# Performance work log

Hardware: AMD Instinct MI355X
Metric: run time of the kernel (lower is better)

## Reference

```python
import jax, jax.numpy as jnp
import numpy as np
from jax import lax

L, C, NH, DFF = 4, 256, 8, 1024
H, W = 56, 56
N = H * W
TOPK, USENUM = 16, 10


def _conv3x3(x, w, b):
    # x: [B,Cin,H,W], w: [Cout,Cin,3,3]
    y = lax.conv_general_dilated(x, w, (1, 1), 'SAME',
                                 dimension_numbers=('NCHW', 'OIHW', 'NCHW'))
    return y + b[None, :, None, None]


def _ln(x, g, b, eps=1e-5):
    m = jnp.mean(x, axis=-1, keepdims=True)
    v = jnp.mean(jnp.square(x - m), axis=-1, keepdims=True)
    return (x - m) * lax.rsqrt(v + eps) * g + b


def _forward(src, conv1_w, conv1_b, conv2_w, conv2_b, near_emb,
             Wq, bq, Wk, bk, Wv, bv, Wo, bo, W1, b1, W2, b2,
             ln1_g, ln1_b, ln2_g, ln2_b, norm_g, norm_b):
    bs, c, h, w = src.shape  # bs == 1 (required by graph_pos broadcasting)
    n = h * w
    nh = NH
    dh = c // nh
    scale = dh ** -0.5

    # conv positional encoder -> per-head sigmoid map
    pe = jax.nn.sigmoid(_conv3x3(jax.nn.relu(_conv3x3(src, conv1_w, conv1_b)),
                                 conv2_w, conv2_b))          # [1,nh,h,w]
    gp = pe.reshape(bs, nh, n)[0].T                          # [n,nh]
    # graph_pos = |pe_i - pe_j| as additive attention bias, [nh,n,n]
    bias = jnp.abs(gp[:, None, :] - gp[None, :, :]).transpose(2, 0, 1)

    x = src.reshape(bs, c, n)[0].T                           # [n,c] tokens
    rows = jnp.arange(n)[:, None]

    for i in range(L):
        # ---- per-layer kNN graph on current features ----
        sq = jnp.sum(x * x, axis=1)
        d2 = sq[:, None] - 2.0 * (x @ x.T) + sq[None, :]     # [n,n] sq dists
        _, idx = lax.top_k(-d2, TOPK)                        # k nearest
        graph = jnp.zeros((n, n), x.dtype).at[rows, idx].set(1.0)
        near = jnp.sum(graph, axis=0)                        # in-degree [n]
        ni = (near / jnp.max(near) * (USENUM - 1)).astype(jnp.int32)
        pos = near_emb[ni]                                   # [n,c] embed gather

        # ---- attention (pos added to q,k; graph_pos biases logits) ----
        qk_in = x + pos
        q = (qk_in @ Wq[i].T + bq[i]).reshape(n, nh, dh)
        k = (qk_in @ Wk[i].T + bk[i]).reshape(n, nh, dh)
        v = (x @ Wv[i].T + bv[i]).reshape(n, nh, dh)
        s = jnp.einsum('ihd,jhd->hij', q * scale, k) + bias  # [nh,n,n]
        att = jax.nn.softmax(s, axis=-1)
        o = jnp.einsum('hij,jhd->ihd', att, v).reshape(n, c) @ Wo[i].T + bo[i]
        x = _ln(x + o, ln1_g[i], ln1_b[i])

        # ---- FFN ----
        ff = jax.nn.relu(x @ W1[i].T + b1[i]) @ W2[i].T + b2[i]
        x = _ln(x + ff, ln2_g[i], ln2_b[i])

    x = _ln(x, norm_g, norm_b)
    return x.T.reshape(bs, c, h, w)


def setup_inputs() -> dict:
    key = jax.random.key(0)
    ks = jax.random.split(key, 20)

    def rn(k, shape, s=0.02):
        return jax.random.normal(k, shape, jnp.float32) * s

    return {
        'src': jax.random.normal(ks[0], (1, C, H, W), jnp.float32),
        'conv1_w': rn(ks[1], (C // 2, C, 3, 3), 0.05),
        'conv1_b': jnp.zeros((C // 2,), jnp.float32),
        'conv2_w': rn(ks[2], (NH, C // 2, 3, 3), 0.05),
        'conv2_b': jnp.zeros((NH,), jnp.float32),
        'near_emb': rn(ks[3], (USENUM, C)),
        'Wq': rn(ks[4], (L, C, C)), 'bq': jnp.zeros((L, C), jnp.float32),
        'Wk': rn(ks[5], (L, C, C)), 'bk': jnp.zeros((L, C), jnp.float32),
        'Wv': rn(ks[6], (L, C, C)), 'bv': jnp.zeros((L, C), jnp.float32),
        'Wo': rn(ks[7], (L, C, C)), 'bo': jnp.zeros((L, C), jnp.float32),
        'W1': rn(ks[8], (L, DFF, C)), 'b1': jnp.zeros((L, DFF), jnp.float32),
        'W2': rn(ks[9], (L, C, DFF)), 'b2': jnp.zeros((L, C), jnp.float32),
        'ln1_g': jnp.ones((L, C), jnp.float32), 'ln1_b': jnp.zeros((L, C), jnp.float32),
        'ln2_g': jnp.ones((L, C), jnp.float32), 'ln2_b': jnp.zeros((L, C), jnp.float32),
        'norm_g': jnp.ones((C,), jnp.float32), 'norm_b': jnp.zeros((C,), jnp.float32),
    }


def reference(src, conv1_w, conv1_b, conv2_w, conv2_b, near_emb,
              Wq, bq, Wk, bk, Wv, bv, Wo, bo, W1, b1, W2, b2,
              ln1_g, ln1_b, ln2_g, ln2_b, norm_g, norm_b):
    return _forward(src, conv1_w, conv1_b, conv2_w, conv2_b, near_emb,
                    Wq, bq, Wk, bk, Wv, bv, Wo, bo, W1, b1, W2, b2,
                    ln1_g, ln1_b, ln2_g, ln2_b, norm_g, norm_b)
```

## Files before the change

kernel.cpp:

```cpp
#include <hip/hip_runtime.h>
#include <math.h>

#define N_TOK 3136
#define CD    256
#define NHD   8
#define DH    32
#define DFFD  1024
#define SCALE 0.17677669529663687f
#define LOG2E 1.4426950408889634f
#define QSC   (SCALE * LOG2E)

typedef __attribute__((ext_vector_type(8))) short short8v;
typedef __attribute__((ext_vector_type(4))) float f32x4;

__device__ __forceinline__ unsigned long long sx64(unsigned long long v, int m) {
  unsigned lo = (unsigned)__shfl_xor((int)(unsigned)(v & 0xffffffffull), m, 64);
  unsigned hi = (unsigned)__shfl_xor((int)(unsigned)(v >> 32), m, 64);
  return ((unsigned long long)hi << 32) | lo;
}

__device__ __forceinline__ unsigned f2mono(float v) {
  unsigned b = __float_as_uint(v);
  return (b & 0x80000000u) ? ~b : (b | 0x80000000u);
}

__device__ __forceinline__ short bfr(float f) {
  unsigned u = __float_as_uint(f);
  unsigned r = (u + 0x7fffu + ((u >> 16) & 1u)) >> 16;
  return (short)r;
}

__device__ __forceinline__ short8v cvt8(float4 a, float4 b) {
  short8v r;
  r[0] = bfr(a.x); r[1] = bfr(a.y); r[2] = bfr(a.z); r[3] = bfr(a.w);
  r[4] = bfr(b.x); r[5] = bfr(b.y); r[6] = bfr(b.z); r[7] = bfr(b.w);
  return r;
}

__global__ __launch_bounds__(256) void transpose_k(const float* __restrict__ in,
    float* __restrict__ out, int R, int C) {
  __shared__ float ls[32][33];
  const int c0 = blockIdx.x * 32, r0 = blockIdx.y * 32;
  const int tx = threadIdx.x & 31, ty = threadIdx.x >> 5;
#pragma unroll
  for (int j = 0; j < 4; ++j) {
    int r = ty + j * 8;
    ls[r][tx] = in[(size_t)(r0 + r) * C + c0 + tx];
  }
  __syncthreads();
#pragma unroll
  for (int j = 0; j < 4; ++j) {
    int cc = ty + j * 8;
    out[(size_t)(c0 + cc) * R + r0 + tx] = ls[tx][cc];
  }
}

__global__ __launch_bounds__(256) void wtr_k(const float* __restrict__ w,
                                             float* __restrict__ wt) {
  const int e = blockIdx.x * 256 + threadIdx.x;
  const int r = e >> 15;
  const int rem = e & 32767;
  const int co = rem >> 8, ci = rem & 255;
  wt[e] = w[((size_t)co * 256 + ci) * 9 + r];
}

__global__ __launch_bounds__(256) void conv1_k(const float* __restrict__ X,
    const float* __restrict__ WT, float* __restrict__ P) {
  __shared__ __align__(16) short As[32][40];
  __shared__ __align__(16) short Bs[64][40];
  const int n0 = blockIdx.x * 64;
  const int m0 = blockIdx.y * 32;
  const int ky = blockIdx.z;
  const int t = threadIdx.x;
  const int w = t >> 6, l = t & 63;
  const int g = l >> 4, c = l & 15;
  const int wr = w >> 1, wc = w & 1;
  const int sr = t >> 2, seg = t & 3;
  const int p = m0 + (sr & 31);
  const int y = p / 56, x = p - y * 56;
  const int yy = y + ky - 1;
  f32x4 acc[2] = {};
  for (int kx = 0; kx < 3; ++kx) {
    const int xx = x + kx - 1;
    const bool valid = (t < 128) && ((unsigned)yy < 56u) && ((unsigned)xx < 56u);
    const float* Ap = X + (size_t)(yy * 56 + xx) * CD + seg * 8;
    const float* Bp = WT + ((size_t)(ky * 3 + kx) * 128 + n0 + sr) * CD + seg * 8;
    for (int k0 = 0; k0 < CD; k0 += 32) {
      float4 a1 = make_float4(0.f, 0.f, 0.f, 0.f), a2 = a1;
      if (valid) { a1 = *(const float4*)(Ap + k0); a2 = *(const float4*)(Ap + k0 + 4); }
      const float4 b1 = *(const float4*)(Bp + k0);
      const float4 b2 = *(const float4*)(Bp + k0 + 4);
      __syncthreads();
      if (t < 128) *(short8v*)&As[sr][seg * 8] = cvt8(a1, a2);
      *(short8v*)&Bs[sr][seg * 8] = cvt8(b1, b2);
      __syncthreads();
      const short8v af = *(const short8v*)&As[wr * 16 + c][g * 8];
      const short8v bf0 = *(const short8v*)&Bs[wc * 32 + c][g * 8];
      const short8v bf1 = *(const short8v*)&Bs[wc * 32 + 16 + c][g * 8];
      acc[0] = __builtin_amdgcn_mfma_f32_16x16x32_bf16(af, bf0, acc[0], 0, 0, 0);
      acc[1] = __builtin_amdgcn_mfma_f32_16x16x32_bf16(af, bf1, acc[1], 0, 0, 0);
    }
  }
#pragma unroll
  for (int ni = 0; ni < 2; ++ni) {
    const int col = n0 + wc * 32 + ni * 16 + c;
#pragma unroll
    for (int q = 0; q < 4; ++q) {
      const int m = m0 + wr * 16 + g * 4 + q;
      P[((size_t)ky * N_TOK + m) * 128 + col] = acc[ni][q];
    }
  }
}

__global__ __launch_bounds__(256) void convred_k(const float* __restrict__ P,
    const float* __restrict__ b, float* __restrict__ T1) {
  const int e = blockIdx.x * 256 + threadIdx.x;
  const float v = P[e] + P[401408 + e] + P[802816 + e] + b[e & 127];
  T1[e] = fmaxf(v, 0.f);
}

template <int RELU>
__global__ __launch_bounds__(256) void gemm32_k(const float* __restrict__ A,
    const float* __restrict__ B, const float* __restrict__ bias,
    float* __restrict__ C, int N, int K) {
  __shared__ __align__(16) short As[32][40];
  __shared__ __align__(16) short Bs[64][40];
  const int n0 = blockIdx.x * 64;
  const int m0 = blockIdx.y * 32;
  const int t = threadIdx.x;
  const int w = t >> 6, l = t & 63;
  const int g = l >> 4, c = l & 15;
  const int wr = w >> 1, wc = w & 1;
  const int sr = t >> 2, seg = t & 3;
  const float* Ap = A + (size_t)(m0 + (sr & 31)) * K + seg * 8;
  const float* Bp = B + (size_t)(n0 + sr) * K + seg * 8;
  f32x4 acc[2] = {};
  for (int k0 = 0; k0 < K; k0 += 32) {
    float4 a1 = make_float4(0.f, 0.f, 0.f, 0.f), a2 = a1;
    if (t < 128) { a1 = *(const float4*)(Ap + k0); a2 = *(const float4*)(Ap + k0 + 4); }
    const float4 b1 = *(const float4*)(Bp + k0);
    const float4 b2 = *(const float4*)(Bp + k0 + 4);
    __syncthreads();
    if (t < 128) *(short8v*)&As[sr][seg * 8] = cvt8(a1, a2);
    *(short8v*)&Bs[sr][seg * 8] = cvt8(b1, b2);
    __syncthreads();
    const short8v af = *(const short8v*)&As[wr * 16 + c][g * 8];
    const short8v bf0 = *(const short8v*)&Bs[wc * 32 + c][g * 8];
    const short8v bf1 = *(const short8v*)&Bs[wc * 32 + 16 + c][g * 8];
    acc[0] = __builtin_amdgcn_mfma_f32_16x16x32_bf16(af, bf0, acc[0], 0, 0, 0);
    acc[1] = __builtin_amdgcn_mfma_f32_16x16x32_bf16(af, bf1, acc[1], 0, 0, 0);
  }
#pragma unroll
  for (int ni = 0; ni < 2; ++ni) {
    const int col = n0 + wc * 32 + ni * 16 + c;
    const float bb = bias ? bias[col] : 0.f;
#pragma unroll
    for (int q = 0; q < 4; ++q) {
      const int m = m0 + wr * 16 + g * 4 + q;
      float v = acc[ni][q] + bb;
      if (RELU) v = fmaxf(v, 0.f);
      C[(size_t)m * N + col] = v;
    }
  }
}

__global__ __launch_bounds__(256) void proj32_k(const float* __restrict__ QKIN,
    const float* __restrict__ X, const float* __restrict__ Wq,
    const float* __restrict__ Wk, const float* __restrict__ Wv,
    const float* __restrict__ bq, const float* __restrict__ bk,
    const float* __restrict__ bv, short* __restrict__ QB,
    short* __restrict__ KB, short* __restrict__ VT) {
  __shared__ __align__(16) short As[32][40];
  __shared__ __align__(16) short Bs[64][40];
  const int sel = blockIdx.z;
  const int n0 = blockIdx.x * 64;
  const int m0 = blockIdx.y * 32;
  const float* A = (sel < 2) ? QKIN : X;
  const float* B = (sel == 0) ? Wq : (sel == 1) ? Wk : Wv;
  const float* bias = (sel == 0) ? bq : (sel == 1) ? bk : bv;
  const int t = threadIdx.x;
  const int w = t >> 6, l = t & 63;
  const int g = l >> 4, c = l & 15;
  const int wr = w >> 1, wc = w & 1;
  const int sr = t >> 2, seg = t & 3;
  const float* Ap = A + (size_t)(m0 + (sr & 31)) * CD + seg * 8;
  const float* Bp = B + (size_t)(n0 + sr) * CD + seg * 8;
  f32x4 acc[2] = {};
  for (int k0 = 0; k0 < CD; k0 += 32) {
    float4 a1 = make_float4(0.f, 0.f, 0.f, 0.f), a2 = a1;
    if (t < 128) { a1 = *(const float4*)(Ap + k0); a2 = *(const float4*)(Ap + k0 + 4); }
    const float4 b1 = *(const float4*)(Bp + k0);
    const float4 b2 = *(const float4*)(Bp + k0 + 4);
    __syncthreads();
    if (t < 128) *(short8v*)&As[sr][seg * 8] = cvt8(a1, a2);
    *(short8v*)&Bs[sr][seg * 8] = cvt8(b1, b2);
    __syncthreads();
    const short8v af = *(const short8v*)&As[wr * 16 + c][g * 8];
    const short8v bf0 = *(const short8v*)&Bs[wc * 32 + c][g * 8];
    const short8v bf1 = *(const short8v*)&Bs[wc * 32 + 16 + c][g * 8];
    acc[0] = __builtin_amdgcn_mfma_f32_16x16x32_bf16(af, bf0, acc[0], 0, 0, 0);
    acc[1] = __builtin_amdgcn_mfma_f32_16x16x32_bf16(af, bf1, acc[1], 0, 0, 0);
  }
#pragma unroll
  for (int ni = 0; ni < 2; ++ni) {
    const int col = n0 + wc * 32 + ni * 16 + c;
    const float bb = bias[col];
    if (sel == 2) {
      const int mb = m0 + wr * 16 + g * 4;
      const int pidx = (mb & ~31) + ((mb >> 4) & 1) * 4 + ((mb >> 2) & 3) * 8;
      uint2 pk;
      const float v0 = acc[ni][0] + bb, v1 = acc[ni][1] + bb;
      const float v2 = acc[ni][2] + bb, v3 = acc[ni][3] + bb;
      pk.x = (unsigned)(unsigned short)bfr(v0) | ((unsigned)(unsigned short)bfr(v1) << 16);
      pk.y = (unsigned)(unsigned short)bfr(v2) | ((unsigned)(unsigned short)bfr(v3) << 16);
      *(uint2*)&VT[(size_t)col * N_TOK + pidx] = pk;
    } else {
      short* Ct = (sel == 0) ? QB : KB;
      const float qs = (sel == 0) ? QSC : 1.f;
      const int hh = col >> 5, dd = col & 31;
#pragma unroll
      for (int q = 0; q < 4; ++q) {
        const int m = m0 + wr * 16 + g * 4 + q;
        Ct[((size_t)hh * N_TOK + m) * 32 + dd] = bfr((acc[ni][q] + bb) * qs);
      }
    }
  }
}

__global__ __launch_bounds__(256) void xsplit_k(const float* __restrict__ X,
    short* __restrict__ XH, short* __restrict__ XL, float* __restrict__ sq) {
  __shared__ float red[4];
  const int i = blockIdx.x, t = threadIdx.x;
  const size_t e = (size_t)i * CD + t;
  const float v = X[e];
  const unsigned ui = __float_as_uint(v);
  XH[e] = (short)(ui >> 16);
  const float hf = __uint_as_float(ui & 0xffff0000u);
  XL[e] = (short)(__float_as_uint(v - hf) >> 16);
  float s = v * v;
#pragma unroll
  for (int m = 1; m < 64; m <<= 1) s += __shfl_xor(s, m, 64);
  if ((t & 63) == 0) red[t >> 6] = s;
  __syncthreads();
  if (t == 0) sq[i] = red[0] + red[1] + red[2] + red[3];
}

__global__ __launch_bounds__(256) void gemm_syr4_k(const short* __restrict__ XH,
    const short* __restrict__ XL, float* __restrict__ C) {
  __shared__ __align__(16) short AsH[64][40];
  __shared__ __align__(16) short AsL[64][40];
  __shared__ __align__(16) short BsH[64][40];
  __shared__ __align__(16) short BsL[64][40];
  int bid = blockIdx.x;
  int bi = (int)((sqrtf(8.f * (float)bid + 1.f) - 1.f) * 0.5f);
  while ((bi + 1) * (bi + 2) / 2 <= bid) ++bi;
  while (bi * (bi + 1) / 2 > bid) --bi;
  const int bj = bid - bi * (bi + 1) / 2;
  const int m0 = bi * 64, n0 = bj * 64;
  const int t = threadIdx.x;
  const int w = t >> 6, l = t & 63;
  const int g = l >> 4, c = l & 15;
  const int wr = w >> 1, wc = w & 1;
  const int sr = t >> 2, seg = t & 3;
  const size_t arow = (size_t)(m0 + sr) * CD + seg * 8;
  const size_t brow = (size_t)(n0 + sr) * CD + seg * 8;
  f32x4 acc[2][2] = {};
  for (int k0 = 0; k0 < CD; k0 += 32) {
    const short8v ah = *(const short8v*)&XH[arow + k0];
    const short8v al = *(const short8v*)&XL[arow + k0];
    const short8v bh = *(const short8v*)&XH[brow + k0];
    const short8v bl = *(const short8v*)&XL[brow + k0];
    __syncthreads();
    *(short8v*)&AsH[sr][seg * 8] = ah;
    *(short8v*)&AsL[sr][seg * 8] = al;
    *(short8v*)&BsH[sr][seg * 8] = bh;
    *(short8v*)&BsL[sr][seg * 8] = bl;
    __syncthreads();
    short8v afH[2], afL[2], bfH[2], bfL[2];
#pragma unroll
    for (int mi = 0; mi < 2; ++mi) {
      afH[mi] = *(const short8v*)&AsH[wr * 32 + mi * 16 + c][g * 8];
      afL[mi] = *(const short8v*)&AsL[wr * 32 + mi * 16 + c][g * 8];
    }
#pragma unroll
    for (int ni = 0; ni < 2; ++ni) {
      bfH[ni] = *(const short8v*)&BsH[wc * 32 + ni * 16 + c][g * 8];
      bfL[ni] = *(const short8v*)&BsL[wc * 32 + ni * 16 + c][g * 8];
    }
#pragma unroll
    for (int mi = 0; mi < 2; ++mi)
#pragma unroll
      for (int ni = 0; ni < 2; ++ni) {
        acc[mi][ni] = __builtin_amdgcn_mfma_f32_16x16x32_bf16(afH[mi], bfH[ni], acc[mi][ni], 0, 0, 0);
        acc[mi][ni] = __builtin_amdgcn_mfma_f32_16x16x32_bf16(afH[mi], bfL[ni], acc[mi][ni], 0, 0, 0);
        acc[mi][ni] = __builtin_amdgcn_mfma_f32_16x16x32_bf16(afL[mi], bfH[ni], acc[mi][ni], 0, 0, 0);
      }
  }
#pragma unroll
  for (int mi = 0; mi < 2; ++mi)
#pragma unroll
    for (int ni = 0; ni < 2; ++ni) {
      const int col = n0 + wc * 32 + ni * 16 + c;
#pragma unroll
      for (int q = 0; q < 4; ++q) {
        const int m = m0 + wr * 32 + mi * 16 + g * 4 + q;
        const float v = acc[mi][ni][q];
        C[(size_t)m * N_TOK + col] = v;
        C[(size_t)col * N_TOK + m] = v;
      }
    }
}

__global__ __launch_bounds__(256) void conv2_k(const float* __restrict__ t1,
    const float* __restrict__ w, const float* __restrict__ b,
    float* __restrict__ gpT) {
  __shared__ float ws3[9 * 8 * 132];
  const int t = threadIdx.x;
  for (int e = t; e < 9216; e += 256) {
    int r = e >> 10;
    int rem = e & 1023;
    int co = rem >> 7;
    int ci = rem & 127;
    ws3[(r * 8 + co) * 132 + ci] = w[((size_t)co * 128 + ci) * 9 + r];
  }
  __syncthreads();
  const int pix = blockIdx.x * 32 + (t >> 3);
  const int co = t & 7;
  const int y = pix / 56, x = pix - y * 56;
  float acc = b[co];
  for (int ky = 0; ky < 3; ++ky) {
    int yy = y + ky - 1;
    if (yy < 0 || yy >= 56) continue;
    for (int kx = 0; kx < 3; ++kx) {
      int xx = x + kx - 1;
      if (xx < 0 || xx >= 56) continue;
      const float4* tp = (const float4*)&t1[(size_t)(yy * 56 + xx) * 128];
      const float* wp = &ws3[((ky * 3 + kx) * 8 + co) * 132];
#pragma unroll
      for (int c4 = 0; c4 < 32; ++c4) {
        const float4 tv = tp[c4];
        const float4 wv = *(const float4*)&wp[c4 * 4];
        acc += tv.x * wv.x + tv.y * wv.y + tv.z * wv.z + tv.w * wv.w;
      }
    }
  }
  gpT[co * N_TOK + pix] = LOG2E / (1.f + expf(-acc));
}

__global__ __launch_bounds__(64) void topk_k(const float* __restrict__ G,
    const float* __restrict__ sq, int* __restrict__ near) {
  const int i = blockIdx.x;
  const int t = threadIdx.x;
  const float sqi = sq[i];
  const float* __restrict__ Grow = G + (size_t)i * N_TOK;
  unsigned cv0 = 0xffffffffu, cv1 = 0xffffffffu, cv2 = 0xffffffffu, cv3 = 0xffffffffu;
  int ce0 = 0, ce1 = 0, ce2 = 0, ce3 = 0;
#pragma unroll
  for (int e = 0; e < 49; ++e) {
    const int j = t + (e << 6);
    const unsigned v = f2mono((sqi - 2.f * Grow[j]) + sq[j]);
    const bool i0 = v < cv0, i1 = v < cv1, i2 = v < cv2, i3 = v < cv3;
    cv3 = i2 ? cv2 : (i3 ? v : cv3);  ce3 = i2 ? ce2 : (i3 ? e : ce3);
    cv2 = i1 ? cv1 : (i2 ? v : cv2);  ce2 = i1 ? ce1 : (i2 ? e : ce2);
    cv1 = i0 ? cv0 : (i1 ? v : cv1);  ce1 = i0 ? ce0 : (i1 ? e : ce1);
    cv0 = i0 ? v : cv0;               ce0 = i0 ? e : ce0;
  }
  unsigned long long killed = 0ull;
#pragma unroll 1
  for (int r = 0; r < 16; ++r) {
    const unsigned long long mine =
        ((unsigned long long)cv0 << 32) | (unsigned)(t + (ce0 << 6));
    unsigned long long best = mine;
#pragma unroll
    for (int m = 1; m < 64; m <<= 1) {
      const unsigned long long o = sx64(best, m);
      best = (o < best) ? o : best;
    }
    if (t == 0) atomicAdd(&near[(unsigned)(best & 0xffffffffu)], 1);
    if (mine == best && r < 15) {
      killed |= 1ull << ce0;
      cv0 = cv1; ce0 = ce1;
      cv1 = cv2; ce1 = ce2;
      cv2 = cv3; ce2 = ce3;
      cv3 = 0xffffffffu; ce3 = 0;
      if (cv0 == 0xffffffffu) {
#pragma unroll
        for (int e = 0; e < 49; ++e) {
          const int j = t + (e << 6);
          unsigned v = f2mono((sqi - 2.f * Grow[j]) + sq[j]);
          v = (((killed >> e) & 1ull) != 0ull) ? 0xffffffffu : v;
          const bool i0 = v < cv0, i1 = v < cv1, i2 = v < cv2, i3 = v < cv3;
          cv3 = i2 ? cv2 : (i3 ? v : cv3);  ce3 = i2 ? ce2 : (i3 ? e : ce3);
          cv2 = i1 ? cv1 : (i2 ? v : cv2);  ce2 = i1 ? ce1 : (i2 ? e : ce2);
          cv1 = i0 ? cv0 : (i1 ? v : cv1);  ce1 = i0 ? ce0 : (i1 ? e : ce1);
          cv0 = i0 ? v : cv0;               ce0 = i0 ? e : ce0;
        }
      }
    }
  }
}

__global__ __launch_bounds__(256) void nearqk_k(const float* __restrict__ x,
    const int* __restrict__ near, const float* __restrict__ emb,
    float* __restrict__ qkin) {
  __shared__ int sm[4];
  const int i = blockIdx.x, t = threadIdx.x;
  int m = 0;
  for (int j = t; j < N_TOK; j += 256) m = max(m, near[j]);
#pragma unroll
  for (int s = 1; s < 64; s <<= 1) m = max(m, __shfl_xor(m, s, 64));
  if ((t & 63) == 0) sm[t >> 6] = m;
  __syncthreads();
  const int mv = max(max(sm[0], sm[1]), max(sm[2], sm[3]));
  const int ni = (int)((float)near[i] / (float)mv * 9.0f);
  qkin[(size_t)i * CD + t] = x[(size_t)i * CD + t] + emb[ni * CD + t];
}

__global__ __launch_bounds__(256) void attn_v7_k(const short* __restrict__ Qb,
    const short* __restrict__ Kb, const short* __restrict__ Vt,
    const float* __restrict__ gpT, float* __restrict__ O1) {
  __shared__ float o_l[4][64][36];
  __shared__ float ml_l[4][64][2];
  const int h = blockIdx.y;
  const int qb = blockIdx.x * 64;
  const int t = threadIdx.x;
  const int w = t >> 6, l = t & 63;
  const int g = l >> 4, c = l & 15;
  const size_t hR = (size_t)h * N_TOK;
  const size_t hoff = (size_t)h * DH;
  short8v qf[4];
  float gpi[4];
#pragma unroll
  for (int gr = 0; gr < 4; ++gr) {
    qf[gr] = *(const short8v*)&Qb[(hR + qb + gr * 16 + c) * 32 + g * 8];
    gpi[gr] = gpT[hR + qb + gr * 16 + c];
  }
  const int jt0 = w ? (13 + 12 * (w - 1)) : 0;
  const int jt1 = jt0 + (w ? 12 : 13);
  float mr[4] = {-INFINITY, -INFINITY, -INFINITY, -INFINITY};
  float lp[4] = {0.f, 0.f, 0.f, 0.f};
  f32x4 oa[4][2] = {};
  const f32x4 zz = {0.f, 0.f, 0.f, 0.f};

#pragma unroll 1
  for (int jt = jt0; jt < jt1; ++jt) {
    const int j0 = jt * 64;
    short8v kf[4], vf[4];
    float4 gj[4];
#pragma unroll
    for (int sub = 0; sub < 4; ++sub)
      kf[sub] = *(const short8v*)&Kb[(hR + j0 + sub * 16 + c) * 32 + g * 8];
#pragma unroll
    for (int ch = 0; ch < 2; ++ch)
#pragma unroll
      for (int ds = 0; ds < 2; ++ds)
        vf[ch * 2 + ds] = *(const short8v*)&Vt[(hoff + ds * 16 + c) * (size_t)N_TOK + j0 + ch * 32 + g * 8];
#pragma unroll
    for (int sub = 0; sub < 4; ++sub)
      gj[sub] = *(const float4*)&gpT[hR + j0 + sub * 16 + g * 4];
#pragma unroll
    for (int gr = 0; gr < 4; ++gr) {
      f32x4 sacc[4];
#pragma unroll
      for (int sub = 0; sub < 4; ++sub)
        sacc[sub] = __builtin_amdgcn_mfma_f32_16x16x32_bf16(kf[sub], qf[gr], zz, 0, 0, 0);
      float sv[16];
#pragma unroll
      for (int sub = 0; sub < 4; ++sub) {
        sv[sub * 4 + 0] = sacc[sub][0] + fabsf(gpi[gr] - gj[sub].x);
        sv[sub * 4 + 1] = sacc[sub][1] + fabsf(gpi[gr] - gj[sub].y);
        sv[sub * 4 + 2] = sacc[sub][2] + fabsf(gpi[gr] - gj[sub].z);
        sv[sub * 4 + 3] = sacc[sub][3] + fabsf(gpi[gr] - gj[sub].w);
      }
      float a0 = fmaxf(sv[0], sv[1]),  a1 = fmaxf(sv[2], sv[3]);
      float a2 = fmaxf(sv[4], sv[5]),  a3 = fmaxf(sv[6], sv[7]);
      float a4 = fmaxf(sv[8], sv[9]),  a5 = fmaxf(sv[10], sv[11]);
      float a6 = fmaxf(sv[12], sv[13]), a7 = fmaxf(sv[14], sv[15]);
      const float mx = fmaxf(fmaxf(fmaxf(a0, a1), fmaxf(a2, a3)),
                             fmaxf(fmaxf(a4, a5), fmaxf(a6, a7)));
      if (!__all(mx - mr[gr] <= 11.f)) {
        float mn = mx;
        mn = fmaxf(mn, __shfl_xor(mn, 16, 64));
        mn = fmaxf(mn, __shfl_xor(mn, 32, 64));
        mn = fmaxf(mn, mr[gr]);
        const float sc = __builtin_amdgcn_exp2f(mr[gr] - mn);
        oa[gr][0][0] *= sc; oa[gr][0][1] *= sc; oa[gr][0][2] *= sc; oa[gr][0][3] *= sc;
        oa[gr][1][0] *= sc; oa[gr][1][1] *= sc; oa[gr][1][2] *= sc; oa[gr][1][3] *= sc;
        lp[gr] *= sc;
        mr[gr] = mn;
      }
      float p[16];
#pragma unroll
      for (int e = 0; e < 16; ++e) p[e] = __builtin_amdgcn_exp2f(sv[e] - mr[gr]);
      const float ps0 = (p[0] + p[1]) + (p[2] + p[3]);
      const float ps1 = (p[4] + p[5]) + (p[6] + p[7]);
      const float ps2 = (p[8] + p[9]) + (p[10] + p[11]);
      const float ps3 = (p[12] + p[13]) + (p[14] + p[15]);
      lp[gr] += (ps0 + ps1) + (ps2 + ps3);
      union { unsigned u[4]; short8v s; } pf0, pf1;
#pragma unroll
      for (int sub = 0; sub < 2; ++sub) {
        pf0.u[2 * sub + 0] = __builtin_amdgcn_perm(__float_as_uint(p[4 * sub + 1]),
                                                   __float_as_uint(p[4 * sub + 0]), 0x07060302u);
        pf0.u[2 * sub + 1] = __builtin_amdgcn_perm(__float_as_uint(p[4 * sub + 3]),
                                                   __float_as_uint(p[4 * sub + 2]), 0x07060302u);
        pf1.u[2 * sub + 0] = __builtin_amdgcn_perm(__float_as_uint(p[8 + 4 * sub + 1]),
                                                   __float_as_uint(p[8 + 4 * sub + 0]), 0x07060302u);
        pf1.u[2 * sub + 1] = __builtin_amdgcn_perm(__float_as_uint(p[8 + 4 * sub + 3]),
                                                   __float_as_uint(p[8 + 4 * sub + 2]), 0x07060302u);
      }
      oa[gr][0] = __builtin_amdgcn_mfma_f32_16x16x32_bf16(vf[0], pf0.s, oa[gr][0], 0, 0, 0);
      oa[gr][1] = __builtin_amdgcn_mfma_f32_16x16x32_bf16(vf[1], pf0.s, oa[gr][1], 0, 0, 0);
      oa[gr][0] = __builtin_amdgcn_mfma_f32_16x16x32_bf16(vf[2], pf1.s, oa[gr][0], 0, 0, 0);
      oa[gr][1] = __builtin_amdgcn_mfma_f32_16x16x32_bf16(vf[3], pf1.s, oa[gr][1], 0, 0, 0);
    }
  }
#pragma unroll
  for (int gr = 0; gr < 4; ++gr) {
    lp[gr] += __shfl_xor(lp[gr], 16, 64);
    lp[gr] += __shfl_xor(lp[gr], 32, 64);
#pragma unroll
    for (int ds = 0; ds < 2; ++ds)
      *(f32x4*)&o_l[w][gr * 16 + c][ds * 16 + g * 4] = oa[gr][ds];
    if (g == 0) {
      ml_l[w][gr * 16 + c][0] = mr[gr];
      ml_l[w][gr * 16 + c][1] = lp[gr];
    }
  }
  __syncthreads();
  const int q = t >> 2, d0 = (t & 3) * 8;
  const float M = fmaxf(fmaxf(ml_l[0][q][0], ml_l[1][q][0]),
                        fmaxf(ml_l[2][q][0], ml_l[3][q][0]));
  float den = 0.f;
  f32x4 numA = {0.f, 0.f, 0.f, 0.f};
  f32x4 numB = {0.f, 0.f, 0.f, 0.f};
#pragma unroll
  for (int sp = 0; sp < 4; ++sp) {
    const float wg = __builtin_amdgcn_exp2f(ml_l[sp][q][0] - M);
    den += wg * ml_l[sp][q][1];
    const f32x4 oA = *(const f32x4*)&o_l[sp][q][d0];
    const f32x4 oB = *(const f32x4*)&o_l[sp][q][d0 + 4];
    numA[0] += wg * oA[0]; numA[1] += wg * oA[1];
    numA[2] += wg * oA[2]; numA[3] += wg * oA[3];
    numB[0] += wg * oB[0]; numB[1] += wg * oB[1];
    numB[2] += wg * oB[2]; numB[3] += wg * oB[3];
  }
  const float inv = 1.f / den;
  f32x4 rA = {numA[0] * inv, numA[1] * inv, numA[2] * inv, numA[3] * inv};
  f32x4 rB = {numB[0] * inv, numB[1] * inv, numB[2] * inv, numB[3] * inv};
  *(f32x4*)&O1[(size_t)(qb + q) * CD + hoff + d0] = rA;
  *(f32x4*)&O1[(size_t)(qb + q) * CD + hoff + d0 + 4] = rB;
}

template <int SPLIT>
__global__ __launch_bounds__(256) void ln_k(const float* __restrict__ xin,
    const float* __restrict__ add, const float* __restrict__ g,
    const float* __restrict__ b, float* __restrict__ xout,
    float* __restrict__ sqout, short* __restrict__ XH, short* __restrict__ XL) {
  __shared__ float red1[4];
  __shared__ float red2[4];
  const int i = blockIdx.x, t = threadIdx.x;
  const size_t e = (size_t)i * CD + t;
  float v = xin[e];
  if (add) v += add[e];
  float s = v;
#pragma unroll
  for (int m = 1; m < 64; m <<= 1) s += __shfl_xor(s, m, 64);
  if ((t & 63) == 0) red1[t >> 6] = s;
  __syncthreads();
  const float mean = (red1[0] + red1[1] + red1[2] + red1[3]) * (1.f / 256.f);
  const float d = v - mean;
  float s2 = d * d;
#pragma unroll
  for (int m = 1; m < 64; m <<= 1) s2 += __shfl_xor(s2, m, 64);
  if ((t & 63) == 0) red2[t >> 6] = s2;
  __syncthreads();
  const float var = (red2[0] + red2[1] + red2[2] + red2[3]) * (1.f / 256.f);
  const float xo = d * rsqrtf(var + 1e-5f) * g[t] + b[t];
  xout[e] = xo;
  if (SPLIT) {
    const unsigned ui = __float_as_uint(xo);
    XH[e] = (short)(ui >> 16);
    const float hf = __uint_as_float(ui & 0xffff0000u);
    XL[e] = (short)(__float_as_uint(xo - hf) >> 16);
    float s3 = xo * xo;
#pragma unroll
    for (int m = 1; m < 64; m <<= 1) s3 += __shfl_xor(s3, m, 64);
    __syncthreads();
    if ((t & 63) == 0) red1[t >> 6] = s3;
    __syncthreads();
    if (t == 0) sqout[i] = red1[0] + red1[1] + red1[2] + red1[3];
  }
}

extern "C" void kernel_launch(void* const* d_in, const int* in_sizes, int n_in,
                              void* d_out, int out_size, void* d_ws, size_t ws_size,
                              hipStream_t stream) {
  const float* src  = (const float*)d_in[0];
  const float* c1w  = (const float*)d_in[1];
  const float* c1b  = (const float*)d_in[2];
  const float* c2w  = (const float*)d_in[3];
  const float* c2b  = (const float*)d_in[4];
  const float* nemb = (const float*)d_in[5];
  const float* Wq   = (const float*)d_in[6];
  const float* bq   = (const float*)d_in[7];
  const float* Wk   = (const float*)d_in[8];
  const float* bk   = (const float*)d_in[9];
  const float* Wv   = (const float*)d_in[10];
  const float* bv   = (const float*)d_in[11];
  const float* Wo   = (const float*)d_in[12];
  const float* bo   = (const float*)d_in[13];
  const float* W1   = (const float*)d_in[14];
  const float* b1   = (const float*)d_in[15];
  const float* W2   = (const float*)d_in[16];
  const float* b2   = (const float*)d_in[17];
  const float* ln1g = (const float*)d_in[18];
  const float* ln1b = (const float*)d_in[19];
  const float* ln2g = (const float*)d_in[20];
  const float* ln2b = (const float*)d_in[21];
  const float* ng   = (const float*)d_in[22];
  const float* nb   = (const float*)d_in[23];

  float* ws = (float*)d_ws;
  const size_t NC = (size_t)N_TOK * CD;
  float* X    = ws;
  float* QKIN = X + NC;
  float* O1   = QKIN + NC;
  float* TMP  = O1 + NC;
  float* FF1  = TMP + NC;
  float* G    = FF1 + (size_t)N_TOK * DFFD;
  float* T1   = G + (size_t)N_TOK * N_TOK;
  float* GPT  = T1 + (size_t)N_TOK * 128;
  float* SQF  = GPT + (size_t)N_TOK * NHD;
  short* QB16 = (short*)(SQF + N_TOK);
  short* KB16 = QB16 + NC;
  short* VT16 = KB16 + NC;
  short* XH   = VT16 + NC;
  short* XL   = XH + NC;
  float* WTC  = (float*)(XL + NC);
  int*   NEAR = (int*)(WTC + 294912);

  transpose_k<<<dim3(98, 8), 256, 0, stream>>>(src, X, 256, N_TOK);
  wtr_k<<<1152, 256, 0, stream>>>(c1w, WTC);
  conv1_k<<<dim3(2, 98, 3), 256, 0, stream>>>(X, WTC, G);
  convred_k<<<1568, 256, 0, stream>>>(G, c1b, T1);
  conv2_k<<<98, 256, 0, stream>>>(T1, c2w, c2b, GPT);
  xsplit_k<<<N_TOK, 256, 0, stream>>>(X, XH, XL, SQF);
  (void)hipMemsetAsync(NEAR, 0, 4 * N_TOK * sizeof(int), stream);

  for (int l = 0; l < 4; ++l) {
    int* NEAR_l = NEAR + l * N_TOK;
    gemm_syr4_k<<<1225, 256, 0, stream>>>(XH, XL, G);
    topk_k<<<N_TOK, 64, 0, stream>>>(G, SQF, NEAR_l);
    nearqk_k<<<N_TOK, 256, 0, stream>>>(X, NEAR_l, nemb, QKIN);
    proj32_k<<<dim3(4, 98, 3), 256, 0, stream>>>(QKIN, X,
        Wq + (size_t)l * 65536, Wk + (size_t)l * 65536, Wv + (size_t)l * 65536,
        bq + l * 256, bk + l * 256, bv + l * 256, QB16, KB16, VT16);
    attn_v7_k<<<dim3(49, 8), 256, 0, stream>>>(QB16, KB16, VT16, GPT, O1);
    gemm32_k<0><<<dim3(4, 98), 256, 0, stream>>>(O1, Wo + (size_t)l * 65536, bo + l * 256, TMP, 256, 256);
    ln_k<0><<<N_TOK, 256, 0, stream>>>(X, TMP, ln1g + l * 256, ln1b + l * 256, X, nullptr, nullptr, nullptr);
    gemm32_k<1><<<dim3(16, 98), 256, 0, stream>>>(X, W1 + (size_t)l * 262144, b1 + l * 1024, FF1, 1024, 256);
    gemm32_k<0><<<dim3(4, 98), 256, 0, stream>>>(FF1, W2 + (size_t)l * 262144, b2 + l * 256, TMP, 256, 1024);
    ln_k<1><<<N_TOK, 256, 0, stream>>>(X, TMP, ln2g + l * 256, ln2b + l * 256, X, SQF, XH, XL);
  }
  ln_k<0><<<N_TOK, 256, 0, stream>>>(X, nullptr, ng, nb, TMP, nullptr, nullptr, nullptr);
  transpose_k<<<dim3(8, 98), 256, 0, stream>>>(TMP, (float*)d_out, N_TOK, 256);
}
```

Measured before the change: 657.1 us.

## Fuse distance-key computation into Gram GEMM and split attention KV over 8 waves

The symmetric Gram GEMM epilogue now computes the squared distance and its monotone integer key directly, so topk only loads precomputed keys instead of recomputing the key from G and sq on every pass. Separately, the attention kernel goes from 4 to 8 waves per block, each handling about half as many KV tiles, with an 8-way merge of partial softmax results. The aim is to cut per-element work in topk and to raise parallelism in the attention kernel, which only launches 392 blocks. The cost is double the shared memory for partials, a larger merge step, and possibly lower occupancy for the 512-thread blocks.

```diff
diff --git a/kernel.cpp b/kernel.cpp
--- a/kernel.cpp
+++ b/kernel.cpp
@@ -246,7 +246,8 @@
 }
 
 __global__ __launch_bounds__(256) void gemm_syr4_k(const short* __restrict__ XH,
-    const short* __restrict__ XL, float* __restrict__ C) {
+    const short* __restrict__ XL, const float* __restrict__ SQ,
+    unsigned* __restrict__ Ck) {
   __shared__ __align__(16) short AsH[64][40];
   __shared__ __align__(16) short AsL[64][40];
   __shared__ __align__(16) short BsH[64][40];
@@ -301,12 +302,14 @@
 #pragma unroll
     for (int ni = 0; ni < 2; ++ni) {
       const int col = n0 + wc * 32 + ni * 16 + c;
+      const float sqc = SQ[col];
 #pragma unroll
       for (int q = 0; q < 4; ++q) {
         const int m = m0 + wr * 32 + mi * 16 + g * 4 + q;
         const float v = acc[mi][ni][q];
-        C[(size_t)m * N_TOK + col] = v;
-        C[(size_t)col * N_TOK + m] = v;
+        const float sqm = SQ[m];
+        Ck[(size_t)m * N_TOK + col] = f2mono((sqm - 2.f * v) + sqc);
+        Ck[(size_t)col * N_TOK + m] = f2mono((sqc - 2.f * v) + sqm);
       }
     }
 }
@@ -347,18 +350,16 @@
   gpT[co * N_TOK + pix] = LOG2E / (1.f + expf(-acc));
 }
 
-__global__ __launch_bounds__(64) void topk_k(const float* __restrict__ G,
-    const float* __restrict__ sq, int* __restrict__ near) {
+__global__ __launch_bounds__(64) void topk_k(const unsigned* __restrict__ Gk,
+    int* __restrict__ near) {
   const int i = blockIdx.x;
   const int t = threadIdx.x;
-  const float sqi = sq[i];
-  const float* __restrict__ Grow = G + (size_t)i * N_TOK;
+  const unsigned* __restrict__ Krow = Gk + (size_t)i * N_TOK;
   unsigned cv0 = 0xffffffffu, cv1 = 0xffffffffu, cv2 = 0xffffffffu, cv3 = 0xffffffffu;
   int ce0 = 0, ce1 = 0, ce2 = 0, ce3 = 0;
 #pragma unroll
   for (int e = 0; e < 49; ++e) {
-    const int j = t + (e << 6);
-    const unsigned v = f2mono((sqi - 2.f * Grow[j]) + sq[j]);
+    const unsigned v = Krow[t + (e << 6)];
     const bool i0 = v < cv0, i1 = v < cv1, i2 = v < cv2, i3 = v < cv3;
     cv3 = i2 ? cv2 : (i3 ? v : cv3);  ce3 = i2 ? ce2 : (i3 ? e : ce3);
     cv2 = i1 ? cv1 : (i2 ? v : cv2);  ce2 = i1 ? ce1 : (i2 ? e : ce2);
@@ -386,8 +387,7 @@
       if (cv0 == 0xffffffffu) {
 #pragma unroll
         for (int e = 0; e < 49; ++e) {
-          const int j = t + (e << 6);
-          unsigned v = f2mono((sqi - 2.f * Grow[j]) + sq[j]);
+          unsigned v = Krow[t + (e << 6)];
           v = (((killed >> e) & 1ull) != 0ull) ? 0xffffffffu : v;
           const bool i0 = v < cv0, i1 = v < cv1, i2 = v < cv2, i3 = v < cv3;
           cv3 = i2 ? cv2 : (i3 ? v : cv3);  ce3 = i2 ? ce2 : (i3 ? e : ce3);
@@ -416,11 +416,11 @@
   qkin[(size_t)i * CD + t] = x[(size_t)i * CD + t] + emb[ni * CD + t];
 }
 
-__global__ __launch_bounds__(256) void attn_v7_k(const short* __restrict__ Qb,
+__global__ __launch_bounds__(512) void attn_v8_k(const short* __restrict__ Qb,
     const short* __restrict__ Kb, const short* __restrict__ Vt,
     const float* __restrict__ gpT, float* __restrict__ O1) {
-  __shared__ float o_l[4][64][36];
-  __shared__ float ml_l[4][64][2];
+  __shared__ float o_l[8][64][36];
+  __shared__ float ml_l[8][64][2];
   const int h = blockIdx.y;
   const int qb = blockIdx.x * 64;
   const int t = threadIdx.x;
@@ -435,8 +435,8 @@
     qf[gr] = *(const short8v*)&Qb[(hR + qb + gr * 16 + c) * 32 + g * 8];
     gpi[gr] = gpT[hR + qb + gr * 16 + c];
   }
-  const int jt0 = w ? (13 + 12 * (w - 1)) : 0;
-  const int jt1 = jt0 + (w ? 12 : 13);
+  const int jt0 = w ? (7 + 6 * (w - 1)) : 0;
+  const int jt1 = jt0 + (w ? 6 : 7);
   float mr[4] = {-INFINITY, -INFINITY, -INFINITY, -INFINITY};
   float lp[4] = {0.f, 0.f, 0.f, 0.f};
   f32x4 oa[4][2] = {};
@@ -528,28 +528,23 @@
     }
   }
   __syncthreads();
-  const int q = t >> 2, d0 = (t & 3) * 8;
-  const float M = fmaxf(fmaxf(ml_l[0][q][0], ml_l[1][q][0]),
-                        fmaxf(ml_l[2][q][0], ml_l[3][q][0]));
+  const int q = t >> 3, d0 = (t & 7) * 4;
+  float M = -INFINITY;
+#pragma unroll
+  for (int sp = 0; sp < 8; ++sp) M = fmaxf(M, ml_l[sp][q][0]);
   float den = 0.f;
-  f32x4 numA = {0.f, 0.f, 0.f, 0.f};
-  f32x4 numB = {0.f, 0.f, 0.f, 0.f};
-#pragma unroll
-  for (int sp = 0; sp < 4; ++sp) {
+  f32x4 num = {0.f, 0.f, 0.f, 0.f};
+#pragma unroll
+  for (int sp = 0; sp < 8; ++sp) {
     const float wg = __builtin_amdgcn_exp2f(ml_l[sp][q][0] - M);
     den += wg * ml_l[sp][q][1];
-    const f32x4 oA = *(const f32x4*)&o_l[sp][q][d0];
-    const f32x4 oB = *(const f32x4*)&o_l[sp][q][d0 + 4];
-    numA[0] += wg * oA[0]; numA[1] += wg * oA[1];
-    numA[2] += wg * oA[2]; numA[3] += wg * oA[3];
-    numB[0] += wg * oB[0]; numB[1] += wg * oB[1];
-    numB[2] += wg * oB[2]; numB[3] += wg * oB[3];
+    const f32x4 ov = *(const f32x4*)&o_l[sp][q][d0];
+    num[0] += wg * ov[0]; num[1] += wg * ov[1];
+    num[2] += wg * ov[2]; num[3] += wg * ov[3];
   }
   const float inv = 1.f / den;
-  f32x4 rA = {numA[0] * inv, numA[1] * inv, numA[2] * inv, numA[3] * inv};
-  f32x4 rB = {numB[0] * inv, numB[1] * inv, numB[2] * inv, numB[3] * inv};
-  *(f32x4*)&O1[(size_t)(qb + q) * CD + hoff + d0] = rA;
-  *(f32x4*)&O1[(size_t)(qb + q) * CD + hoff + d0 + 4] = rB;
+  f32x4 r = {num[0] * inv, num[1] * inv, num[2] * inv, num[3] * inv};
+  *(f32x4*)&O1[(size_t)(qb + q) * CD + hoff + d0] = r;
 }
 
 template <int SPLIT>
@@ -650,13 +645,13 @@
 
   for (int l = 0; l < 4; ++l) {
     int* NEAR_l = NEAR + l * N_TOK;
-    gemm_syr4_k<<<1225, 256, 0, stream>>>(XH, XL, G);
-    topk_k<<<N_TOK, 64, 0, stream>>>(G, SQF, NEAR_l);
+    gemm_syr4_k<<<1225, 256, 0, stream>>>(XH, XL, SQF, (unsigned*)G);
+    topk_k<<<N_TOK, 64, 0, stream>>>((const unsigned*)G, NEAR_l);
     nearqk_k<<<N_TOK, 256, 0, stream>>>(X, NEAR_l, nemb, QKIN);
     proj32_k<<<dim3(4, 98, 3), 256, 0, stream>>>(QKIN, X,
         Wq + (size_t)l * 65536, Wk + (size_t)l * 65536, Wv + (size_t)l * 65536,
         bq + l * 256, bk + l * 256, bv + l * 256, QB16, KB16, VT16);
-    attn_v7_k<<<dim3(49, 8), 256, 0, stream>>>(QB16, KB16, VT16, GPT, O1);
+    attn_v8_k<<<dim3(49, 8), 512, 0, stream>>>(QB16, KB16, VT16, GPT, O1);
     gemm32_k<0><<<dim3(4, 98), 256, 0, stream>>>(O1, Wo + (size_t)l * 65536, bo + l * 256, TMP, 256, 256);
     ln_k<0><<<N_TOK, 256, 0, stream>>>(X, TMP, ln1g + l * 256, ln1b + l * 256, X, nullptr, nullptr, nullptr);
     gemm32_k<1><<<dim3(16, 98), 256, 0, stream>>>(X, W1 + (size_t)l * 262144, b1 + l * 1024, FF1, 1024, 256);
```

Result: faster. 641.1 us (-2.4%).
